# Performance work log

Hardware: AMD Instinct MI355X
Metric: run time of the kernel (lower is better)

## Reference

```python
import jax, jax.numpy as jnp
import numpy as np

N_NODES = 30000


def rgcn_layer(h, src, dst, etype, norm, coeff_l, basis_l, bias_l):
    """One basis-decomposed RelGraphConv layer (sum aggregation, relu)."""
    # W: [R, d, d] from basis decomposition
    W = jnp.einsum('rb,bdk->rdk', coeff_l, basis_l)
    # Per-relation transform of all nodes: [R, N, d] (same math as per-edge h[src] @ W[etype])
    H = jnp.einsum('nd,rdk->rnk', h, W)
    msg = H[etype, src] * norm          # [E, d]
    agg = jax.ops.segment_sum(msg, dst, num_segments=N_NODES)
    return jax.nn.relu(agg + bias_l)


def encode(feats, src, dst, etype, norm, coeff, basis, bias):
    h = feats
    for l in range(coeff.shape[0]):
        h = rgcn_layer(h, src, dst, etype, norm, coeff[l], basis[l], bias[l])
    return h


def setup_inputs() -> dict:
    key = jax.random.key(0)
    ks = jax.random.split(key, 20)
    d, R, B, L = 128, 32, 8, 2
    E, P = 480000, 100000
    inp = {
        'p_feats': jax.random.normal(ks[0], (N_NODES, d), jnp.float32),
        'n_feats': jax.random.normal(ks[1], (N_NODES, d), jnp.float32),
        'w_relation': jax.random.normal(ks[2], (16, d), jnp.float32),
        'coeff': jax.random.normal(ks[3], (L, R, B), jnp.float32) / np.sqrt(B),
        'basis': jax.random.normal(ks[4], (L, B, d, d), jnp.float32) / np.sqrt(d),
        'bias': jnp.zeros((L, d), jnp.float32),
        'p_src': jax.random.randint(ks[5], (E,), 0, N_NODES, jnp.int32),
        'p_dst': jax.random.randint(ks[6], (E,), 0, N_NODES, jnp.int32),
        'p_etype': jax.random.randint(ks[7], (E,), 0, R, jnp.int32),
        'p_norm': jax.random.uniform(ks[8], (E, 1), jnp.float32),
        'n_src': jax.random.randint(ks[9], (E,), 0, N_NODES, jnp.int32),
        'n_dst': jax.random.randint(ks[10], (E,), 0, N_NODES, jnp.int32),
        'n_etype': jax.random.randint(ks[11], (E,), 0, R, jnp.int32),
        'n_norm': jax.random.uniform(ks[12], (E, 1), jnp.float32),
        'pg_head': jax.random.randint(ks[13], (P,), 0, N_NODES, jnp.int32),
        'pg_tail': jax.random.randint(ks[14], (P,), 0, N_NODES, jnp.int32),
        'pg_etype': jax.random.randint(ks[15], (P,), 0, 16, jnp.int32),
        'ng_head': jax.random.randint(ks[16], (P,), 0, N_NODES, jnp.int32),
        'ng_tail': jax.random.randint(ks[17], (P,), 0, N_NODES, jnp.int32),
    }
    return inp


def reference(p_feats, n_feats, w_relation, coeff, basis, bias,
              p_src, p_dst, p_etype, p_norm,
              n_src, n_dst, n_etype, n_norm,
              pg_head, pg_tail, pg_etype, ng_head, ng_tail):
    p_h = encode(p_feats, p_src, p_dst, p_etype, p_norm, coeff, basis, bias)
    n_h = encode(n_feats, n_src, n_dst, n_etype, n_norm, coeff, basis, bias)
    p_head_emb = p_h[pg_head]
    p_tail_emb = p_h[pg_tail]
    r_emb = w_relation[pg_etype]
    n_head_emb = n_h[ng_head]
    n_tail_emb = n_h[ng_tail]
    return (p_head_emb, p_tail_emb, r_emb, n_head_emb, n_tail_emb, p_h, n_h)
```

## Files before the change

### kernel.cpp

```cpp
#include <hip/hip_runtime.h>

typedef __attribute__((ext_vector_type(8))) short short8;
typedef __attribute__((ext_vector_type(4))) float f32x4;

#define DIM 128
#define RREL 32
#define BB 8

__device__ __forceinline__ ushort f2bf(float f) {
    unsigned u = __builtin_bit_cast(unsigned, f);
    u = (u + 0x7FFFu + ((u >> 16) & 1u)) >> 16;
    return (ushort)u;
}
__device__ __forceinline__ float bf2f(unsigned u) {
    return __builtin_bit_cast(float, u << 16);
}

__global__ __launch_bounds__(256) void prep_kernel(const float* __restrict__ basis,
                                                   ushort* __restrict__ Bt,
                                                   const float* __restrict__ f0,
                                                   const float* __restrict__ f1,
                                                   ushort* __restrict__ hb, int nnd,
                                                   int fblocks) {
    int bid = blockIdx.x;
    int t = threadIdx.x;
    if (bid < 32) {
        __shared__ ushort ld[32][258];
        int l = bid >> 4, sub = bid & 15;
        int n0 = (sub >> 2) * 32, k0 = (sub & 3) * 256;
        const float* bs = basis + (size_t)l * BB * DIM * DIM;
#pragma unroll 4
        for (int it = 0; it < 32; ++it) {
            int idx = it * 256 + t;
            int nn = idx & 31, kd = idx >> 5;
            int kg = k0 + kd;
            ld[nn][kd] = f2bf(bs[(size_t)(kg >> 7) * DIM * DIM + (kg & 127) * DIM + n0 + nn]);
        }
        __syncthreads();
        ushort* ob = Bt + (size_t)l * DIM * 1024;
#pragma unroll 4
        for (int it = 0; it < 32; ++it) {
            ob[(size_t)(n0 + it) * 1024 + k0 + t] = ld[it][t];
        }
    } else {
        int fb = bid - 32;
        int g = fb / fblocks;
        int i = (fb - g * fblocks) * 256 + t;
        int n8 = nnd / 8;
        if (i >= n8) return;
        const float* in = g ? f1 : f0;
        ushort* out = hb + (size_t)g * nnd;
        const float4* p = (const float4*)in + 2 * (size_t)i;
        float4 a = p[0], b = p[1];
        unsigned w0 = f2bf(a.x) | ((unsigned)f2bf(a.y) << 16);
        unsigned w1 = f2bf(a.z) | ((unsigned)f2bf(a.w) << 16);
        unsigned w2 = f2bf(b.x) | ((unsigned)f2bf(b.y) << 16);
        unsigned w3 = f2bf(b.z) | ((unsigned)f2bf(b.w) << 16);
        ((uint4*)out)[i] = make_uint4(w0, w1, w2, w3);
    }
}

__global__ __launch_bounds__(256) void histd_kernel(const int* __restrict__ dst, int E,
                                                    int* __restrict__ dh) {
    for (int i = blockIdx.x * 256 + threadIdx.x; i < E; i += gridDim.x * 256)
        atomicAdd(&dh[dst[i]], 1);
}

__global__ __launch_bounds__(1024) void dscan_kernel(const int* __restrict__ dh, int NN, int E,
                                                     int* __restrict__ doff,
                                                     int* __restrict__ dcur) {
    __shared__ int part[1024];
    int t = threadIdx.x;
    int chunk = (NN + 1023) >> 10;
    int b0 = t * chunk, b1 = b0 + chunk;
    if (b0 > NN) b0 = NN;
    if (b1 > NN) b1 = NN;
    int s = 0;
    for (int i = b0; i < b1; ++i) s += dh[i];
    part[t] = s;
    __syncthreads();
    for (int off = 1; off < 1024; off <<= 1) {
        int v = (t >= off) ? part[t - off] : 0;
        __syncthreads();
        part[t] += v;
        __syncthreads();
    }
    int run = part[t] - s;
    for (int i = b0; i < b1; ++i) {
        doff[i] = run; dcur[i] = run; run += dh[i];
    }
    if (t == 0) doff[NN] = E;
}

__global__ __launch_bounds__(256) void dstsort_kernel(const int* __restrict__ src,
                                                      const int* __restrict__ dst,
                                                      const int* __restrict__ et,
                                                      const float* __restrict__ norm, int E,
                                                      int* __restrict__ dcur,
                                                      int4* __restrict__ epack) {
    int i = blockIdx.x * 256 + threadIdx.x;
    if (i >= E) return;
    int p = atomicAdd(&dcur[dst[i]], 1);
    epack[p] = make_int4(src[i], et[i], __builtin_bit_cast(int, norm[i]), 0);
}

__global__ __launch_bounds__(256) void ustep_kernel(const ushort* __restrict__ hb,
                                                    const float* __restrict__ coeff,
                                                    const int4* __restrict__ epack,
                                                    const int* __restrict__ doff,
                                                    ushort* __restrict__ U, int NN) {
    __shared__ float cb[RREL * BB];
    int t = threadIdx.x;
    if (t < RREL * BB) cb[t] = coeff[t];
    __syncthreads();
    int d = blockIdx.x * 4 + (t >> 6);
    if (d >= NN) return;
    int lane = t & 63;
    int s0 = doff[d], s1 = doff[d + 1];
    float a0[BB], a1[BB];
#pragma unroll
    for (int b = 0; b < BB; ++b) { a0[b] = 0.f; a1[b] = 0.f; }
    int j = s0;
    for (; j + 1 < s1; j += 2) {
        int4 eA = epack[j], eB = epack[j + 1];
        unsigned hA = ((const unsigned*)(hb + (size_t)eA.x * DIM))[lane];
        unsigned hB = ((const unsigned*)(hb + (size_t)eB.x * DIM))[lane];
        float nA = __builtin_bit_cast(float, eA.z), nB = __builtin_bit_cast(float, eB.z);
        float xA = bf2f(hA & 0xffffu), yA = bf2f(hA >> 16);
        float xB = bf2f(hB & 0xffffu), yB = bf2f(hB >> 16);
        const float* cA = cb + eA.y * BB;
        const float* cB = cb + eB.y * BB;
#pragma unroll
        for (int b = 0; b < BB; ++b) {
            float wA = cA[b] * nA, wB = cB[b] * nB;
            a0[b] = fmaf(wA, xA, fmaf(wB, xB, a0[b]));
            a1[b] = fmaf(wA, yA, fmaf(wB, yB, a1[b]));
        }
    }
    if (j < s1) {
        int4 eA = epack[j];
        unsigned hA = ((const unsigned*)(hb + (size_t)eA.x * DIM))[lane];
        float nA = __builtin_bit_cast(float, eA.z);
        float xA = bf2f(hA & 0xffffu), yA = bf2f(hA >> 16);
        const float* cA = cb + eA.y * BB;
#pragma unroll
        for (int b = 0; b < BB; ++b) {
            float wA = cA[b] * nA;
            a0[b] = fmaf(wA, xA, a0[b]);
            a1[b] = fmaf(wA, yA, a1[b]);
        }
    }
    unsigned* Ur = (unsigned*)(U + (size_t)d * 1024);
#pragma unroll
    for (int b = 0; b < BB; ++b)
        Ur[b * 64 + lane] = (unsigned)f2bf(a0[b]) | ((unsigned)f2bf(a1[b]) << 16);
}

__global__ __launch_bounds__(512) void ugemm_kernel(const ushort* __restrict__ U,
                                                    const ushort* __restrict__ Bt,
                                                    const float* __restrict__ bias,
                                                    float* __restrict__ of32,
                                                    ushort* __restrict__ obf, int NN) {
    __shared__ ushort lds[2][2][DIM][64];
    int t = threadIdx.x;
    int row0 = blockIdx.x * 128;
    int w = t >> 6, l = t & 63;
    int wr = w >> 2, wc = w & 3;
    int lr16 = l & 15, lhi = l >> 4;

    int r_row[2], r_sw[2];
    const ushort* aptr[2];
    const ushort* bptr[2];
#pragma unroll
    for (int i = 0; i < 2; ++i) {
        int g = i * 512 + t;
        int row = g >> 3, ci = g & 7;
        r_row[i] = row; r_sw[i] = ci ^ (row & 7);
        int ar = row0 + row; if (ar > NN - 1) ar = NN - 1;
        aptr[i] = U + (size_t)ar * 1024 + ci * 8;
        bptr[i] = Bt + (size_t)row * 1024 + ci * 8;
    }

    f32x4 acc[4][2];
#pragma unroll
    for (int m = 0; m < 4; ++m)
#pragma unroll
        for (int n = 0; n < 2; ++n) acc[m][n] = (f32x4)0.f;

    int4 ra[2], rb[2];
#pragma unroll
    for (int i = 0; i < 2; ++i) { ra[i] = *(const int4*)aptr[i]; rb[i] = *(const int4*)bptr[i]; }
#pragma unroll
    for (int i = 0; i < 2; ++i) {
        ((int4*)&lds[0][0][r_row[i]][0])[r_sw[i]] = ra[i];
        ((int4*)&lds[0][1][r_row[i]][0])[r_sw[i]] = rb[i];
    }
    __syncthreads();

    for (int kk = 0; kk < 16; ++kk) {
        if (kk < 15) {
#pragma unroll
            for (int i = 0; i < 2; ++i) {
                ra[i] = *(const int4*)(aptr[i] + (kk + 1) * 64);
                rb[i] = *(const int4*)(bptr[i] + (kk + 1) * 64);
            }
        }
        const short8* As = (const short8*)&lds[kk & 1][0][0][0];
        const short8* Bs = (const short8*)&lds[kk & 1][1][0][0];
#pragma unroll
        for (int k4 = 0; k4 < 2; ++k4) {
            int kc = k4 * 4 + lhi;
            short8 a[4];
#pragma unroll
            for (int m = 0; m < 4; ++m) {
                int ar = wr * 64 + m * 16 + lr16;
                a[m] = As[ar * 8 + (kc ^ (ar & 7))];
            }
#pragma unroll
            for (int n16 = 0; n16 < 2; ++n16) {
                int n = wc * 32 + n16 * 16 + lr16;
                short8 b = Bs[n * 8 + (kc ^ (n & 7))];
#pragma unroll
                for (int m = 0; m < 4; ++m)
                    acc[m][n16] = __builtin_amdgcn_mfma_f32_16x16x32_bf16(a[m], b, acc[m][n16], 0, 0, 0);
            }
        }
        if (kk < 15) {
            int nb = (kk + 1) & 1;
#pragma unroll
            for (int i = 0; i < 2; ++i) {
                ((int4*)&lds[nb][0][r_row[i]][0])[r_sw[i]] = ra[i];
                ((int4*)&lds[nb][1][r_row[i]][0])[r_sw[i]] = rb[i];
            }
        }
        __syncthreads();
    }

    if (of32) {
#pragma unroll
        for (int m = 0; m < 4; ++m)
#pragma unroll
            for (int j = 0; j < 4; ++j) {
                int row = wr * 64 + m * 16 + lhi * 4 + j;
                if (row0 + row < NN) {
#pragma unroll
                    for (int n16 = 0; n16 < 2; ++n16) {
                        int col = wc * 32 + n16 * 16 + lr16;
                        float v = fmaxf(acc[m][n16][j] + bias[col], 0.f);
                        of32[(size_t)(row0 + row) * DIM + col] = v;
                    }
                }
            }
    } else {
        ushort* Cl = (ushort*)lds;
#pragma unroll
        for (int m = 0; m < 4; ++m)
#pragma unroll
            for (int j = 0; j < 4; ++j) {
                int row = wr * 64 + m * 16 + lhi * 4 + j;
#pragma unroll
                for (int n16 = 0; n16 < 2; ++n16) {
                    int col = wc * 32 + n16 * 16 + lr16;
                    float v = fmaxf(acc[m][n16][j] + bias[col], 0.f);
                    Cl[(row * 128 + col) ^ ((row & 7) << 3)] = f2bf(v);
                }
            }
        __syncthreads();
        const int4* Cv = (const int4*)lds;
#pragma unroll
        for (int i2 = 0; i2 < 4; ++i2) {
            int idx = i2 * 512 + t;
            int row = idx >> 4, ci = idx & 15;
            if (row0 + row < NN) {
                int4 v = Cv[(row * 16 + ci) ^ (row & 7)];
                ((int4*)(obf + (size_t)(row0 + row) * DIM))[ci] = v;
            }
        }
    }
}

__global__ __launch_bounds__(256) void gather_kernel(const float* __restrict__ p_h,
                                                     const float* __restrict__ n_h,
                                                     const float* __restrict__ w_rel,
                                                     const int* __restrict__ pg_head,
                                                     const int* __restrict__ pg_tail,
                                                     const int* __restrict__ pg_et,
                                                     const int* __restrict__ ng_head,
                                                     const int* __restrict__ ng_tail,
                                                     float* __restrict__ out, int P) {
    long tid = (long)blockIdx.x * 256 + threadIdx.x;
    long total = (long)5 * P * 32;
    if (tid >= total) return;
    int c = (int)(tid & 31);
    long rest = tid >> 5;
    int i = (int)(rest % P);
    int which = (int)(rest / P);
    const float* srcp; int row;
    switch (which) {
        case 0: srcp = p_h;   row = pg_head[i]; break;
        case 1: srcp = p_h;   row = pg_tail[i]; break;
        case 2: srcp = w_rel; row = pg_et[i];   break;
        case 3: srcp = n_h;   row = ng_head[i]; break;
        default: srcp = n_h;  row = ng_tail[i]; break;
    }
    float4 v = ((const float4*)(srcp + (size_t)row * DIM))[c];
    ((float4*)out)[((size_t)which * P + i) * 32 + c] = v;
}

extern "C" void kernel_launch(void* const* d_in, const int* in_sizes, int n_in,
                              void* d_out, int out_size, void* d_ws, size_t ws_size,
                              hipStream_t stream) {
    const float* feats[2] = {(const float*)d_in[0], (const float*)d_in[1]};
    const float* w_relation = (const float*)d_in[2];
    const float* coeff = (const float*)d_in[3];
    const float* basis = (const float*)d_in[4];
    const float* bias = (const float*)d_in[5];
    const int* srcs[2] = {(const int*)d_in[6], (const int*)d_in[10]};
    const int* dsts[2] = {(const int*)d_in[7], (const int*)d_in[11]};
    const int* ets[2] = {(const int*)d_in[8], (const int*)d_in[12]};
    const float* norms[2] = {(const float*)d_in[9], (const float*)d_in[13]};
    const int* pg_head = (const int*)d_in[14];
    const int* pg_tail = (const int*)d_in[15];
    const int* pg_et = (const int*)d_in[16];
    const int* ng_head = (const int*)d_in[17];
    const int* ng_tail = (const int*)d_in[18];

    int E = in_sizes[6];
    int P = in_sizes[14];
    int NN = in_sizes[0] / DIM;
    int nnd = NN * DIM;
    float* out = (float*)d_out;

    char* w = (char*)d_ws;
    auto alloc = [&](size_t b) { char* p = w; w += (b + 255) & ~(size_t)255; return p; };

    ushort* Bt = (ushort*)alloc((size_t)2 * DIM * 1024 * 2);
    ushort* hb = (ushort*)alloc((size_t)2 * nnd * 2);
    ushort* hb2 = (ushort*)alloc((size_t)nnd * 2);
    int4* epack = (int4*)alloc((size_t)E * 16);
    int* dhist = (int*)alloc((size_t)NN * 4);
    int* dcur = (int*)alloc((size_t)NN * 4);
    int* doff = (int*)alloc((size_t)(NN + 1) * 4);
    ushort* U = (ushort*)alloc((size_t)NN * 1024 * 2);

    int fblocks = (nnd / 8 + 255) / 256;
    prep_kernel<<<32 + 2 * fblocks, 256, 0, stream>>>(basis, Bt, feats[0], feats[1], hb, nnd,
                                                      fblocks);

    int gblocks = (NN + 127) / 128;
    for (int g = 0; g < 2; ++g) {
        float* hout = out + (size_t)5 * P * DIM + (size_t)g * nnd;
        hipMemsetAsync(dhist, 0, (size_t)NN * 4, stream);
        histd_kernel<<<512, 256, 0, stream>>>(dsts[g], E, dhist);
        dscan_kernel<<<1, 1024, 0, stream>>>(dhist, NN, E, doff, dcur);
        dstsort_kernel<<<(E + 255) / 256, 256, 0, stream>>>(srcs[g], dsts[g], ets[g], norms[g],
                                                            E, dcur, epack);
        for (int l = 0; l < 2; ++l) {
            ustep_kernel<<<(NN + 3) / 4, 256, 0, stream>>>(
                l ? hb2 : hb + (size_t)g * nnd, coeff + l * RREL * BB, epack, doff, U, NN);
            ugemm_kernel<<<gblocks, 512, 0, stream>>>(
                U, Bt + (size_t)l * DIM * 1024, bias + l * DIM, l ? hout : nullptr,
                l ? nullptr : hb2, NN);
        }
    }

    const float* p_h = out + (size_t)5 * P * DIM;
    const float* n_h = p_h + (size_t)NN * DIM;
    long gtotal = (long)5 * P * 32;
    gather_kernel<<<(int)((gtotal + 255) / 256), 256, 0, stream>>>(
        p_h, n_h, w_relation, pg_head, pg_tail, pg_et, ng_head, ng_tail, out, P);
}
```

Baseline: 834.1 us.

## Fuse edge aggregation with basis GEMM and batch both graphs' preprocessing

Aggregation of basis-weighted neighbour features is now fused with the basis GEMM in one kernel. Each 32-row tile is built in LDS instead of being written to and re-read from a global U buffer (30000x1024 bf16 per layer). The histogram, scan and dst-sort steps for both graphs are merged into single launches, and the histogram is folded into the prep kernel, which cuts launches and serialization. The trade-off is large LDS per block (about 80KB), lower occupancy, and B tiles reloaded per 32-row block rather than per 128 rows.

```diff
diff --git a/kernel.cpp b/kernel.cpp
--- a/kernel.cpp
+++ b/kernel.cpp
@@ -21,7 +21,11 @@
                                                    const float* __restrict__ f0,
                                                    const float* __restrict__ f1,
                                                    ushort* __restrict__ hb, int nnd,
-                                                   int fblocks) {
+                                                   int fblocks,
+                                                   const int* __restrict__ dst0,
+                                                   const int* __restrict__ dst1,
+                                                   int* __restrict__ dh0,
+                                                   int* __restrict__ dh1, int E) {
     int bid = blockIdx.x;
     int t = threadIdx.x;
     if (bid < 32) {
@@ -42,7 +46,7 @@
         for (int it = 0; it < 32; ++it) {
             ob[(size_t)(n0 + it) * 1024 + k0 + t] = ld[it][t];
         }
-    } else {
+    } else if (bid < 32 + 2 * fblocks) {
         int fb = bid - 32;
         int g = fb / fblocks;
         int i = (fb - g * fblocks) * 256 + t;
@@ -57,19 +61,26 @@
         unsigned w2 = f2bf(b.x) | ((unsigned)f2bf(b.y) << 16);
         unsigned w3 = f2bf(b.z) | ((unsigned)f2bf(b.w) << 16);
         ((uint4*)out)[i] = make_uint4(w0, w1, w2, w3);
-    }
-}
-
-__global__ __launch_bounds__(256) void histd_kernel(const int* __restrict__ dst, int E,
-                                                    int* __restrict__ dh) {
-    for (int i = blockIdx.x * 256 + threadIdx.x; i < E; i += gridDim.x * 256)
-        atomicAdd(&dh[dst[i]], 1);
-}
-
-__global__ __launch_bounds__(1024) void dscan_kernel(const int* __restrict__ dh, int NN, int E,
-                                                     int* __restrict__ doff,
-                                                     int* __restrict__ dcur) {
+    } else {
+        int hbid = bid - (32 + 2 * fblocks);
+        int g = hbid >> 9;
+        int b = hbid & 511;
+        const int* dp = g ? dst1 : dst0;
+        int* dh = g ? dh1 : dh0;
+        for (int i = b * 256 + t; i < E; i += 512 * 256) atomicAdd(&dh[dp[i]], 1);
+    }
+}
+
+__global__ __launch_bounds__(1024) void dscan2_kernel(const int* __restrict__ dh0,
+                                                      const int* __restrict__ dh1, int NN, int E,
+                                                      int* __restrict__ doff0,
+                                                      int* __restrict__ dcur0,
+                                                      int* __restrict__ doff1,
+                                                      int* __restrict__ dcur1) {
     __shared__ int part[1024];
+    const int* dh = blockIdx.x ? dh1 : dh0;
+    int* doff = blockIdx.x ? doff1 : doff0;
+    int* dcur = blockIdx.x ? dcur1 : dcur0;
     int t = threadIdx.x;
     int chunk = (NN + 1023) >> 10;
     int b0 = t * chunk, b1 = b0 + chunk;
@@ -92,189 +103,153 @@
     if (t == 0) doff[NN] = E;
 }
 
-__global__ __launch_bounds__(256) void dstsort_kernel(const int* __restrict__ src,
-                                                      const int* __restrict__ dst,
-                                                      const int* __restrict__ et,
-                                                      const float* __restrict__ norm, int E,
-                                                      int* __restrict__ dcur,
-                                                      int4* __restrict__ epack) {
+__global__ __launch_bounds__(256) void dstsort2_kernel(
+    const int* __restrict__ s0, const int* __restrict__ d0, const int* __restrict__ e0,
+    const float* __restrict__ n0, const int* __restrict__ s1, const int* __restrict__ d1,
+    const int* __restrict__ e1, const float* __restrict__ n1, int E,
+    int* __restrict__ dcur0, int* __restrict__ dcur1,
+    int4* __restrict__ ep0, int4* __restrict__ ep1) {
     int i = blockIdx.x * 256 + threadIdx.x;
-    if (i >= E) return;
+    const int* src; const int* dst; const int* et; const float* nm;
+    int* dcur; int4* ep;
+    if (i < E) {
+        src = s0; dst = d0; et = e0; nm = n0; dcur = dcur0; ep = ep0;
+    } else {
+        i -= E;
+        if (i >= E) return;
+        src = s1; dst = d1; et = e1; nm = n1; dcur = dcur1; ep = ep1;
+    }
     int p = atomicAdd(&dcur[dst[i]], 1);
-    epack[p] = make_int4(src[i], et[i], __builtin_bit_cast(int, norm[i]), 0);
-}
-
-__global__ __launch_bounds__(256) void ustep_kernel(const ushort* __restrict__ hb,
-                                                    const float* __restrict__ coeff,
-                                                    const int4* __restrict__ epack,
-                                                    const int* __restrict__ doff,
-                                                    ushort* __restrict__ U, int NN) {
-    __shared__ float cb[RREL * BB];
+    ep[p] = make_int4(src[i], et[i], __builtin_bit_cast(int, nm[i]), 0);
+}
+
+__global__ __launch_bounds__(512) void fused_layer_kernel(
+    const ushort* __restrict__ hbsrc, const float* __restrict__ coeff,
+    const int4* __restrict__ epack, const int* __restrict__ doff,
+    const ushort* __restrict__ Bt, const float* __restrict__ bias,
+    float* __restrict__ of32, ushort* __restrict__ obf, int NN) {
+    __shared__ ushort Ul[32 * 1024];
+    __shared__ ushort Bl[128 * 64];
+
     int t = threadIdx.x;
+    int w = t >> 6, lane = t & 63;
+    int row0 = blockIdx.x * 32;
+
+    float* cb = (float*)Bl;
     if (t < RREL * BB) cb[t] = coeff[t];
     __syncthreads();
-    int d = blockIdx.x * 4 + (t >> 6);
-    if (d >= NN) return;
-    int lane = t & 63;
-    int s0 = doff[d], s1 = doff[d + 1];
-    float a0[BB], a1[BB];
-#pragma unroll
-    for (int b = 0; b < BB; ++b) { a0[b] = 0.f; a1[b] = 0.f; }
-    int j = s0;
-    for (; j + 1 < s1; j += 2) {
-        int4 eA = epack[j], eB = epack[j + 1];
-        unsigned hA = ((const unsigned*)(hb + (size_t)eA.x * DIM))[lane];
-        unsigned hB = ((const unsigned*)(hb + (size_t)eB.x * DIM))[lane];
-        float nA = __builtin_bit_cast(float, eA.z), nB = __builtin_bit_cast(float, eB.z);
-        float xA = bf2f(hA & 0xffffu), yA = bf2f(hA >> 16);
-        float xB = bf2f(hB & 0xffffu), yB = bf2f(hB >> 16);
-        const float* cA = cb + eA.y * BB;
-        const float* cB = cb + eB.y * BB;
+
+    unsigned* Uw = (unsigned*)Ul;
+    int kkb = lane >> 5;
+    int cisw = (lane >> 2) & 7;
+    int lo = lane & 3;
+#pragma unroll
+    for (int i = 0; i < 4; ++i) {
+        int row = w * 4 + i;
+        int d = row0 + row;
+        int s0 = 0, s1 = 0;
+        if (d < NN) { s0 = doff[d]; s1 = doff[d + 1]; }
+        float a0[BB], a1[BB];
+#pragma unroll
+        for (int b = 0; b < BB; ++b) { a0[b] = 0.f; a1[b] = 0.f; }
+        int j = s0;
+        for (; j + 3 < s1; j += 4) {
+            int4 eA = epack[j], eB = epack[j + 1], eC = epack[j + 2], eD = epack[j + 3];
+            unsigned hA = ((const unsigned*)(hbsrc + (size_t)eA.x * DIM))[lane];
+            unsigned hB = ((const unsigned*)(hbsrc + (size_t)eB.x * DIM))[lane];
+            unsigned hC = ((const unsigned*)(hbsrc + (size_t)eC.x * DIM))[lane];
+            unsigned hD = ((const unsigned*)(hbsrc + (size_t)eD.x * DIM))[lane];
+            float nA = __builtin_bit_cast(float, eA.z), nB = __builtin_bit_cast(float, eB.z);
+            float nC = __builtin_bit_cast(float, eC.z), nD = __builtin_bit_cast(float, eD.z);
+            float xA = bf2f(hA & 0xffffu), yA = bf2f(hA >> 16);
+            float xB = bf2f(hB & 0xffffu), yB = bf2f(hB >> 16);
+            float xC = bf2f(hC & 0xffffu), yC = bf2f(hC >> 16);
+            float xD = bf2f(hD & 0xffffu), yD = bf2f(hD >> 16);
+            const float* cA = cb + (eA.y << 3);
+            const float* cB = cb + (eB.y << 3);
+            const float* cC = cb + (eC.y << 3);
+            const float* cD = cb + (eD.y << 3);
+#pragma unroll
+            for (int b = 0; b < BB; ++b) {
+                float wA = cA[b] * nA, wB = cB[b] * nB, wC = cC[b] * nC, wD = cD[b] * nD;
+                a0[b] = fmaf(wA, xA, fmaf(wB, xB, fmaf(wC, xC, fmaf(wD, xD, a0[b]))));
+                a1[b] = fmaf(wA, yA, fmaf(wB, yB, fmaf(wC, yC, fmaf(wD, yD, a1[b]))));
+            }
+        }
+        for (; j < s1; ++j) {
+            int4 eA = epack[j];
+            unsigned hA = ((const unsigned*)(hbsrc + (size_t)eA.x * DIM))[lane];
+            float nA = __builtin_bit_cast(float, eA.z);
+            float xA = bf2f(hA & 0xffffu), yA = bf2f(hA >> 16);
+            const float* cA = cb + (eA.y << 3);
+#pragma unroll
+            for (int b = 0; b < BB; ++b) {
+                float wA = cA[b] * nA;
+                a0[b] = fmaf(wA, xA, a0[b]);
+                a1[b] = fmaf(wA, yA, a1[b]);
+            }
+        }
+        int sw = cisw ^ (row & 7);
 #pragma unroll
         for (int b = 0; b < BB; ++b) {
-            float wA = cA[b] * nA, wB = cB[b] * nB;
-            a0[b] = fmaf(wA, xA, fmaf(wB, xB, a0[b]));
-            a1[b] = fmaf(wA, yA, fmaf(wB, yB, a1[b]));
-        }
-    }
-    if (j < s1) {
-        int4 eA = epack[j];
-        unsigned hA = ((const unsigned*)(hb + (size_t)eA.x * DIM))[lane];
-        float nA = __builtin_bit_cast(float, eA.z);
-        float xA = bf2f(hA & 0xffffu), yA = bf2f(hA >> 16);
-        const float* cA = cb + eA.y * BB;
-#pragma unroll
-        for (int b = 0; b < BB; ++b) {
-            float wA = cA[b] * nA;
-            a0[b] = fmaf(wA, xA, a0[b]);
-            a1[b] = fmaf(wA, yA, a1[b]);
-        }
-    }
-    unsigned* Ur = (unsigned*)(U + (size_t)d * 1024);
-#pragma unroll
-    for (int b = 0; b < BB; ++b)
-        Ur[b * 64 + lane] = (unsigned)f2bf(a0[b]) | ((unsigned)f2bf(a1[b]) << 16);
-}
-
-__global__ __launch_bounds__(512) void ugemm_kernel(const ushort* __restrict__ U,
-                                                    const ushort* __restrict__ Bt,
-                                                    const float* __restrict__ bias,
-                                                    float* __restrict__ of32,
-                                                    ushort* __restrict__ obf, int NN) {
-    __shared__ ushort lds[2][2][DIM][64];
-    int t = threadIdx.x;
-    int row0 = blockIdx.x * 128;
-    int w = t >> 6, l = t & 63;
-    int wr = w >> 2, wc = w & 3;
-    int lr16 = l & 15, lhi = l >> 4;
-
-    int r_row[2], r_sw[2];
-    const ushort* aptr[2];
-    const ushort* bptr[2];
-#pragma unroll
-    for (int i = 0; i < 2; ++i) {
-        int g = i * 512 + t;
-        int row = g >> 3, ci = g & 7;
-        r_row[i] = row; r_sw[i] = ci ^ (row & 7);
-        int ar = row0 + row; if (ar > NN - 1) ar = NN - 1;
-        aptr[i] = U + (size_t)ar * 1024 + ci * 8;
-        bptr[i] = Bt + (size_t)row * 1024 + ci * 8;
-    }
-
-    f32x4 acc[4][2];
-#pragma unroll
-    for (int m = 0; m < 4; ++m)
-#pragma unroll
-        for (int n = 0; n < 2; ++n) acc[m][n] = (f32x4)0.f;
-
-    int4 ra[2], rb[2];
-#pragma unroll
-    for (int i = 0; i < 2; ++i) { ra[i] = *(const int4*)aptr[i]; rb[i] = *(const int4*)bptr[i]; }
-#pragma unroll
-    for (int i = 0; i < 2; ++i) {
-        ((int4*)&lds[0][0][r_row[i]][0])[r_sw[i]] = ra[i];
-        ((int4*)&lds[0][1][r_row[i]][0])[r_sw[i]] = rb[i];
+            int kk = b * 2 + kkb;
+            Uw[row * 512 + kk * 32 + sw * 4 + lo] =
+                (unsigned)f2bf(a0[b]) | ((unsigned)f2bf(a1[b]) << 16);
+        }
     }
     __syncthreads();
 
+    int lr16 = lane & 15, lhi = lane >> 4;
+    f32x4 acc0 = (f32x4)0.f, acc1 = (f32x4)0.f;
+    int4* BlV = (int4*)Bl;
+    const short8* As = (const short8*)Ul;
+    const short8* Bs = (const short8*)Bl;
+    int bn = w * 16 + lr16;
     for (int kk = 0; kk < 16; ++kk) {
-        if (kk < 15) {
-#pragma unroll
-            for (int i = 0; i < 2; ++i) {
-                ra[i] = *(const int4*)(aptr[i] + (kk + 1) * 64);
-                rb[i] = *(const int4*)(bptr[i] + (kk + 1) * 64);
-            }
-        }
-        const short8* As = (const short8*)&lds[kk & 1][0][0][0];
-        const short8* Bs = (const short8*)&lds[kk & 1][1][0][0];
-#pragma unroll
-        for (int k4 = 0; k4 < 2; ++k4) {
-            int kc = k4 * 4 + lhi;
-            short8 a[4];
-#pragma unroll
-            for (int m = 0; m < 4; ++m) {
-                int ar = wr * 64 + m * 16 + lr16;
-                a[m] = As[ar * 8 + (kc ^ (ar & 7))];
-            }
-#pragma unroll
-            for (int n16 = 0; n16 < 2; ++n16) {
-                int n = wc * 32 + n16 * 16 + lr16;
-                short8 b = Bs[n * 8 + (kc ^ (n & 7))];
-#pragma unroll
-                for (int m = 0; m < 4; ++m)
-                    acc[m][n16] = __builtin_amdgcn_mfma_f32_16x16x32_bf16(a[m], b, acc[m][n16], 0, 0, 0);
-            }
-        }
-        if (kk < 15) {
-            int nb = (kk + 1) & 1;
-#pragma unroll
-            for (int i = 0; i < 2; ++i) {
-                ((int4*)&lds[nb][0][r_row[i]][0])[r_sw[i]] = ra[i];
-                ((int4*)&lds[nb][1][r_row[i]][0])[r_sw[i]] = rb[i];
-            }
-        }
-        __syncthreads();
-    }
-
+#pragma unroll
+        for (int i = 0; i < 2; ++i) {
+            int g = i * 512 + t;
+            int n = g >> 3, ci = g & 7;
+            BlV[n * 8 + (ci ^ (n & 7))] =
+                ((const int4*)(Bt + (size_t)n * 1024 + kk * 64))[ci];
+        }
+        __syncthreads();
+#pragma unroll
+        for (int ks = 0; ks < 2; ++ks) {
+            int kc = ks * 4 + lhi;
+            short8 b = Bs[bn * 8 + (kc ^ (bn & 7))];
+            short8 am0 = As[(0 * 16 + lr16) * 128 + kk * 8 + (kc ^ ((0 * 16 + lr16) & 7))];
+            short8 am1 = As[(1 * 16 + lr16) * 128 + kk * 8 + (kc ^ ((1 * 16 + lr16) & 7))];
+            acc0 = __builtin_amdgcn_mfma_f32_16x16x32_bf16(am0, b, acc0, 0, 0, 0);
+            acc1 = __builtin_amdgcn_mfma_f32_16x16x32_bf16(am1, b, acc1, 0, 0, 0);
+        }
+        __syncthreads();
+    }
+
+    float bv = bias[bn];
     if (of32) {
 #pragma unroll
-        for (int m = 0; m < 4; ++m)
-#pragma unroll
-            for (int j = 0; j < 4; ++j) {
-                int row = wr * 64 + m * 16 + lhi * 4 + j;
-                if (row0 + row < NN) {
-#pragma unroll
-                    for (int n16 = 0; n16 < 2; ++n16) {
-                        int col = wc * 32 + n16 * 16 + lr16;
-                        float v = fmaxf(acc[m][n16][j] + bias[col], 0.f);
-                        of32[(size_t)(row0 + row) * DIM + col] = v;
-                    }
-                }
-            }
+        for (int j = 0; j < 4; ++j) {
+            int r0 = lhi * 4 + j;
+            int r1 = 16 + r0;
+            if (row0 + r0 < NN) of32[(size_t)(row0 + r0) * DIM + bn] = fmaxf(acc0[j] + bv, 0.f);
+            if (row0 + r1 < NN) of32[(size_t)(row0 + r1) * DIM + bn] = fmaxf(acc1[j] + bv, 0.f);
+        }
     } else {
-        ushort* Cl = (ushort*)lds;
-#pragma unroll
-        for (int m = 0; m < 4; ++m)
-#pragma unroll
-            for (int j = 0; j < 4; ++j) {
-                int row = wr * 64 + m * 16 + lhi * 4 + j;
-#pragma unroll
-                for (int n16 = 0; n16 < 2; ++n16) {
-                    int col = wc * 32 + n16 * 16 + lr16;
-                    float v = fmaxf(acc[m][n16][j] + bias[col], 0.f);
-                    Cl[(row * 128 + col) ^ ((row & 7) << 3)] = f2bf(v);
-                }
-            }
-        __syncthreads();
-        const int4* Cv = (const int4*)lds;
-#pragma unroll
-        for (int i2 = 0; i2 < 4; ++i2) {
-            int idx = i2 * 512 + t;
-            int row = idx >> 4, ci = idx & 15;
-            if (row0 + row < NN) {
-                int4 v = Cv[(row * 16 + ci) ^ (row & 7)];
-                ((int4*)(obf + (size_t)(row0 + row) * DIM))[ci] = v;
-            }
+        ushort* Cl = (ushort*)Bl;
+#pragma unroll
+        for (int j = 0; j < 4; ++j) {
+            int r0 = lhi * 4 + j;
+            int r1 = 16 + r0;
+            Cl[(r0 * 128 + bn) ^ ((r0 & 7) << 3)] = f2bf(fmaxf(acc0[j] + bv, 0.f));
+            Cl[(r1 * 128 + bn) ^ ((r1 & 7) << 3)] = f2bf(fmaxf(acc1[j] + bv, 0.f));
+        }
+        __syncthreads();
+        const int4* Cv = (const int4*)Bl;
+        int row = t >> 4, ci = t & 15;
+        if (row0 + row < NN) {
+            int4 v = Cv[(row * 16 + ci) ^ (row & 7)];
+            ((int4*)(obf + (size_t)(row0 + row) * DIM))[ci] = v;
         }
     }
 }
@@ -337,35 +312,42 @@
     ushort* Bt = (ushort*)alloc((size_t)2 * DIM * 1024 * 2);
     ushort* hb = (ushort*)alloc((size_t)2 * nnd * 2);
     ushort* hb2 = (ushort*)alloc((size_t)nnd * 2);
-    int4* epack = (int4*)alloc((size_t)E * 16);
-    int* dhist = (int*)alloc((size_t)NN * 4);
-    int* dcur = (int*)alloc((size_t)NN * 4);
-    int* doff = (int*)alloc((size_t)(NN + 1) * 4);
-    ushort* U = (ushort*)alloc((size_t)NN * 1024 * 2);
+    int4* ep0 = (int4*)alloc((size_t)E * 16);
+    int4* ep1 = (int4*)alloc((size_t)E * 16);
+    int* dh0 = (int*)alloc((size_t)NN * 4);
+    int* dh1 = (int*)alloc((size_t)NN * 4);
+    int* dcur0 = (int*)alloc((size_t)NN * 4);
+    int* dcur1 = (int*)alloc((size_t)NN * 4);
+    int* doff0 = (int*)alloc((size_t)(NN + 1) * 4);
+    int* doff1 = (int*)alloc((size_t)(NN + 1) * 4);
+
+    float* p_h = out + (size_t)5 * P * DIM;
+    float* n_h = p_h + (size_t)nnd;
+
+    hipMemsetAsync(dh0, 0, ((char*)dh1 + (size_t)NN * 4) - (char*)dh0, stream);
 
     int fblocks = (nnd / 8 + 255) / 256;
-    prep_kernel<<<32 + 2 * fblocks, 256, 0, stream>>>(basis, Bt, feats[0], feats[1], hb, nnd,
-                                                      fblocks);
-
-    int gblocks = (NN + 127) / 128;
-    for (int g = 0; g < 2; ++g) {
-        float* hout = out + (size_t)5 * P * DIM + (size_t)g * nnd;
-        hipMemsetAsync(dhist, 0, (size_t)NN * 4, stream);
-        histd_kernel<<<512, 256, 0, stream>>>(dsts[g], E, dhist);
-        dscan_kernel<<<1, 1024, 0, stream>>>(dhist, NN, E, doff, dcur);
-        dstsort_kernel<<<(E + 255) / 256, 256, 0, stream>>>(srcs[g], dsts[g], ets[g], norms[g],
-                                                            E, dcur, epack);
-        for (int l = 0; l < 2; ++l) {
-            ustep_kernel<<<(NN + 3) / 4, 256, 0, stream>>>(
-                l ? hb2 : hb + (size_t)g * nnd, coeff + l * RREL * BB, epack, doff, U, NN);
-            ugemm_kernel<<<gblocks, 512, 0, stream>>>(
-                U, Bt + (size_t)l * DIM * 1024, bias + l * DIM, l ? hout : nullptr,
-                l ? nullptr : hb2, NN);
-        }
-    }
-
-    const float* p_h = out + (size_t)5 * P * DIM;
-    const float* n_h = p_h + (size_t)NN * DIM;
+    prep_kernel<<<32 + 2 * fblocks + 1024, 256, 0, stream>>>(
+        basis, Bt, feats[0], feats[1], hb, nnd, fblocks, dsts[0], dsts[1], dh0, dh1, E);
+
+    dscan2_kernel<<<2, 1024, 0, stream>>>(dh0, dh1, NN, E, doff0, dcur0, doff1, dcur1);
+
+    dstsort2_kernel<<<(2 * E + 255) / 256, 256, 0, stream>>>(
+        srcs[0], dsts[0], ets[0], norms[0], srcs[1], dsts[1], ets[1], norms[1], E,
+        dcur0, dcur1, ep0, ep1);
+
+    int gblocks = (NN + 31) / 32;
+    fused_layer_kernel<<<gblocks, 512, 0, stream>>>(hb, coeff, ep0, doff0, Bt, bias,
+                                                    nullptr, hb2, NN);
+    fused_layer_kernel<<<gblocks, 512, 0, stream>>>(hb2, coeff + RREL * BB, ep0, doff0,
+                                                    Bt + (size_t)DIM * 1024, bias + DIM,
+                                                    p_h, nullptr, NN);
+    fused_layer_kernel<<<gblocks, 512, 0, stream>>>(hb + (size_t)nnd, coeff, ep1, doff1, Bt,
+                                                    bias, nullptr, hb2, NN);
+    fused_layer_kernel<<<gblocks, 512, 0, stream>>>(hb2, coeff + RREL * BB, ep1, doff1,
+                                                    Bt + (size_t)DIM * 1024, bias + DIM,
+                                                    n_h, nullptr, NN);
+
     long gtotal = (long)5 * P * 32;
     gather_kernel<<<(int)((gtotal + 255) / 256), 256, 0, stream>>>(
         p_h, n_h, w_relation, pg_head, pg_tail, pg_et, ng_head, ng_tail, out, P);
```

Result: faster. 804.4 us (-3.6%).
